# Optimization experiments

Measured on AMD Instinct MI355X. Metric: run time of the kernel, lower is better.

## Reference

```python
import jax, jax.numpy as jnp
import numpy as np

# constants mirroring init_kwargs
SPATIAL_STRIDE = 4
RADIUS2 = 0.5 ** 2
K = 32


def _fps(xyz, m):
    """Iterative farthest point sampling. xyz: [N,3] -> idx [m] int32 (starts at index 0, like pointnet2)."""
    n = xyz.shape[0]

    def body(i, carry):
        dist, idx = carry
        cur = xyz[idx[i]]                              # [3]
        d = jnp.sum((xyz - cur) ** 2, axis=-1)          # [N]
        dist = jnp.minimum(dist, d)
        idx = idx.at[i + 1].set(jnp.argmax(dist).astype(jnp.int32))
        return dist, idx

    dist0 = jnp.full((n,), 1e10, xyz.dtype)
    idx0 = jnp.zeros((m,), jnp.int32)
    _, idx = jax.lax.fori_loop(0, m - 1, body, (dist0, idx0))
    return idx


def setup_inputs() -> dict:
    key = jax.random.key(0)
    ks = jax.random.split(key, 5)
    B, T, N, C = 4, 8, 2048, 64
    C_IN = 2 * C + 3  # grouped feat2 + anchor feat1 + xyz displacement
    xyzs = jax.random.uniform(ks[0], (B, T, N, 3), dtype=jnp.float32)
    features = jax.random.normal(ks[1], (B, T, N, C), dtype=jnp.float32)
    w1 = jax.random.normal(ks[2], (C_IN, 128), dtype=jnp.float32) / np.sqrt(C_IN)
    w2 = jax.random.normal(ks[3], (128, 128), dtype=jnp.float32) / np.sqrt(128)
    w3 = jax.random.normal(ks[4], (128, 256), dtype=jnp.float32) / np.sqrt(128)
    return {
        "xyzs": xyzs, "features": features,
        "w1": w1, "b1": jnp.zeros((128,), jnp.float32),
        "w2": w2, "b2": jnp.zeros((128,), jnp.float32),
        "w3": w3, "b3": jnp.zeros((256,), jnp.float32),
    }


def reference(xyzs, features, w1, b1, w2, b2, w3, b3):
    B, T, N, _ = xyzs.shape
    M = N // SPATIAL_STRIDE

    # temporal replicate padding [1,1]
    xp = jnp.concatenate([xyzs[:, :1], xyzs, xyzs[:, -1:]], axis=1)        # [B,T+2,N,3]
    fp = jnp.concatenate([features[:, :1], features, features[:, -1:]], axis=1)
    # frames processed: i = 1..T (stride 1); neighbor frame = i+1
    xyz_a, xyz_n = xp[:, 1:T + 1], xp[:, 2:T + 2]                          # [B,T,N,3]
    feat_a, feat_n = fp[:, 1:T + 1], fp[:, 2:T + 2]                        # [B,T,N,C]

    gather = jax.vmap(jax.vmap(lambda a, i: a[i]))  # over (B, T)

    # FPS on each anchor frame
    idx = jax.vmap(jax.vmap(lambda p: _fps(p, M)))(xyz_a)                  # [B,T,M]
    anchor = gather(xyz_a, idx)                                            # [B,T,M,3]
    f1 = gather(feat_a, idx)                                               # [B,T,M,C]

    # knn of anchors into next frame, with ball-query radius clamp
    d = jnp.sum((anchor[:, :, :, None, :] - xyz_n[:, :, None, :, :]) ** 2, axis=-1)  # [B,T,M,N]
    negd, idxk = jax.lax.top_k(-d, K)                                      # [B,T,M,K]
    idxk = jnp.where(-negd <= RADIUS2, idxk, idxk[..., :1])                # duplicate nearest outside radius

    gxyz = gather(xyz_n, idxk)                                             # [B,T,M,K,3]
    gf2 = gather(feat_n, idxk)                                             # [B,T,M,K,C]
    disp = gxyz - anchor[:, :, :, None, :]
    h = jnp.concatenate(
        [gf2, jnp.broadcast_to(f1[:, :, :, None, :], gf2.shape), disp], axis=-1)  # [B,T,M,K,2C+3]

    h = jax.nn.relu(h @ w1 + b1)
    h = jax.nn.relu(h @ w2 + b2)
    h = jax.nn.relu(h @ w3 + b3)
    new_features = jnp.max(h, axis=3)                                      # [B,T,M,256]
    return anchor, new_features
```

## Files before the change

### kernel.cpp

```cpp
#include <hip/hip_runtime.h>

#define BB 4
#define TT 8
#define NN 2048
#define CC 64
#define MM 512
#define KK 32
#define H3DIM 256
#define RAD2 0.25f
#define FINF 3.4e38f

typedef _Float16 f16x8 __attribute__((ext_vector_type(8)));
typedef _Float16 f16x4 __attribute__((ext_vector_type(4)));
typedef float f32x4 __attribute__((ext_vector_type(4)));

template <int CTRL>
__device__ __forceinline__ float dpp_max_step(float x) {
    int xi = __builtin_bit_cast(int, x);
    int yi = __builtin_amdgcn_update_dpp(xi, xi, CTRL, 0xf, 0xf, false);
    return fmaxf(x, __builtin_bit_cast(float, yi));
}
__device__ __forceinline__ float wave_max64(float x) {
    x = dpp_max_step<0x111>(x);
    x = dpp_max_step<0x112>(x);
    x = dpp_max_step<0x114>(x);
    x = dpp_max_step<0x118>(x);
    x = dpp_max_step<0x142>(x);
    x = dpp_max_step<0x143>(x);
    return __builtin_bit_cast(float, __builtin_amdgcn_readlane(__builtin_bit_cast(int, x), 63));
}
template <int CTRL>
__device__ __forceinline__ unsigned long long dpp_minkey_step(unsigned long long k) {
    int lo = (int)(unsigned)k;
    int hi = (int)(unsigned)(k >> 32);
    int slo = __builtin_amdgcn_update_dpp(lo, lo, CTRL, 0xf, 0xf, false);
    int shi = __builtin_amdgcn_update_dpp(hi, hi, CTRL, 0xf, 0xf, false);
    unsigned long long s = ((unsigned long long)(unsigned)shi << 32) | (unsigned)slo;
    return s < k ? s : k;
}
__device__ __forceinline__ unsigned long long wave_minkey(unsigned long long k) {
    k = dpp_minkey_step<0x111>(k);
    k = dpp_minkey_step<0x112>(k);
    k = dpp_minkey_step<0x114>(k);
    k = dpp_minkey_step<0x118>(k);
    k = dpp_minkey_step<0x142>(k);
    k = dpp_minkey_step<0x143>(k);
    int lo = __builtin_amdgcn_readlane((int)(unsigned)k, 63);
    int hi = __builtin_amdgcn_readlane((int)(unsigned)(k >> 32), 63);
    return ((unsigned long long)(unsigned)hi << 32) | (unsigned)lo;
}

__global__ __launch_bounds__(256) void k_fps(const float* __restrict__ xyzs,
                                             int* __restrict__ fps_idx) {
    int bt = blockIdx.x;
    int tid = threadIdx.x;
    int lane = tid & 63, w = tid >> 6;
    __shared__ float sx[NN], sy[NN], sz[NN];
    __shared__ float4 rec_xyzd[2][4];
    __shared__ __align__(16) int rec_p[2][4];
    const float* src = xyzs + (size_t)bt * NN * 3;
    for (int i = tid; i < NN; i += 256) {
        sx[i] = src[i * 3 + 0];
        sy[i] = src[i * 3 + 1];
        sz[i] = src[i * 3 + 2];
    }
    __syncthreads();

    float px[8], py[8], pz[8], dist[8];
#pragma unroll
    for (int j = 0; j < 8; ++j) {
        int p = tid * 8 + j;
        px[j] = sx[p]; py[j] = sy[p]; pz[j] = sz[p];
        dist[j] = 1e10f;
    }

    if (tid == 0) fps_idx[bt * MM + 0] = 0;
    int pbase = tid * 8;
    float cx = sx[0], cy = sy[0], cz = sz[0];

    for (int it = 1; it < MM; ++it) {
        float nd[8];
#pragma unroll
        for (int j = 0; j < 8; ++j) {
            float dx = px[j] - cx, dy = py[j] - cy, dz = pz[j] - cz;
            float d = dx * dx + dy * dy + dz * dz;
            nd[j] = fminf(dist[j], d);
            dist[j] = nd[j];
        }
        float gd0 = nd[0]; int gj0 = 0;
#pragma unroll
        for (int j = 1; j < 4; ++j) if (nd[j] > gd0) { gd0 = nd[j]; gj0 = j; }
        float gd1 = nd[4]; int gj1 = 4;
#pragma unroll
        for (int j = 5; j < 8; ++j) if (nd[j] > gd1) { gd1 = nd[j]; gj1 = j; }
        bool gt = gd1 > gd0;
        float bestd = gt ? gd1 : gd0;
        int bestj = gt ? gj1 : gj0;
        int bestp = pbase + bestj;
        float wmax = wave_max64(bestd);
        unsigned long long mask = __ballot(bestd == wmax);
        int wl = __ffsll(mask) - 1;
        int wbp = __builtin_amdgcn_readlane(bestp, wl);
        if (lane == wl) {
            bool b0 = (bestj & 1) != 0, b1 = (bestj & 2) != 0, b2 = (bestj & 4) != 0;
            float x01 = b0 ? px[1] : px[0], x23 = b0 ? px[3] : px[2];
            float x45 = b0 ? px[5] : px[4], x67 = b0 ? px[7] : px[6];
            float y01 = b0 ? py[1] : py[0], y23 = b0 ? py[3] : py[2];
            float y45 = b0 ? py[5] : py[4], y67 = b0 ? py[7] : py[6];
            float z01 = b0 ? pz[1] : pz[0], z23 = b0 ? pz[3] : pz[2];
            float z45 = b0 ? pz[5] : pz[4], z67 = b0 ? pz[7] : pz[6];
            float x0123 = b1 ? x23 : x01, x4567 = b1 ? x67 : x45;
            float y0123 = b1 ? y23 : y01, y4567 = b1 ? y67 : y45;
            float z0123 = b1 ? z23 : z01, z4567 = b1 ? z67 : z45;
            float4 r;
            r.x = b2 ? x4567 : x0123;
            r.y = b2 ? y4567 : y0123;
            r.z = b2 ? z4567 : z0123;
            r.w = wmax;
            rec_xyzd[it & 1][w] = r;
        }
        if (lane == 0) rec_p[it & 1][w] = wbp;
        __syncthreads();
        float4 r0 = rec_xyzd[it & 1][0];
        float4 r1 = rec_xyzd[it & 1][1];
        float4 r2 = rec_xyzd[it & 1][2];
        float4 r3 = rec_xyzd[it & 1][3];
        int4 pv = *(const int4*)&rec_p[it & 1][0];
        bool t01 = r1.w > r0.w, t23 = r3.w > r2.w;
        float4 ra = t01 ? r1 : r0; int pa = t01 ? pv.y : pv.x;
        float4 rb = t23 ? r3 : r2; int pb = t23 ? pv.w : pv.z;
        bool tf = rb.w > ra.w;
        float4 rf = tf ? rb : ra;
        int pf = tf ? pb : pa;
        cx = rf.x; cy = rf.y; cz = rf.z;
        if (tid == 0) fps_idx[bt * MM + it] = pf;
    }
}

__global__ __launch_bounds__(256) void k_pp(const float* __restrict__ xyzs,
                                            const float* __restrict__ feats,
                                            const float* __restrict__ w1,
                                            _Float16* __restrict__ Pp) {
    __shared__ float sw[68 * 128];
    __shared__ float sin_[64 * 68];
    int tid = threadIdx.x;
    for (int i = tid; i < 68 * 128; i += 256) {
        int r = i >> 7, c = i & 127;
        float v = 0.f;
        if (r < 64) v = w1[r * 128 + c];
        else if (r < 67) v = w1[(128 + r - 64) * 128 + c];
        sw[i] = v;
    }
    int row0 = blockIdx.x * 64;
    int bt = row0 >> 11;
    int b = bt >> 3, t = bt & 7;
    int tn = (t + 1 < TT) ? (t + 1) : (TT - 1);
    size_t nbase = (size_t)(b * TT + tn) * NN + (row0 & (NN - 1));
    const float* fsrc = feats + nbase * CC;
    const float* xsrc = xyzs + nbase * 3;
    for (int i = tid; i < 1024; i += 256) {
        float4 v = ((const float4*)fsrc)[i];
        int r = i >> 4, c = (i & 15) * 4;
        *(float4*)&sin_[r * 68 + c] = v;
    }
    if (tid < 192) {
        int r = tid / 3, c = tid - r * 3;
        sin_[r * 68 + 64 + c] = xsrc[tid];
    }
    if (tid < 64) sin_[tid * 68 + 67] = 0.f;
    __syncthreads();

    int rowg = tid >> 5, colg = tid & 31;
    float4 acc[8];
#pragma unroll
    for (int i = 0; i < 8; ++i) acc[i] = make_float4(0.f, 0.f, 0.f, 0.f);
    for (int k = 0; k < 68; k += 4) {
        float4 a4[8], b4[4];
#pragma unroll
        for (int i = 0; i < 8; ++i) a4[i] = *(const float4*)&sin_[(rowg * 8 + i) * 68 + k];
#pragma unroll
        for (int kk = 0; kk < 4; ++kk) b4[kk] = *(const float4*)&sw[(k + kk) * 128 + colg * 4];
#pragma unroll
        for (int i = 0; i < 8; ++i) {
#pragma unroll
            for (int kk = 0; kk < 4; ++kk) {
                float av = (kk == 0) ? a4[i].x : (kk == 1) ? a4[i].y : (kk == 2) ? a4[i].z : a4[i].w;
                acc[i].x += av * b4[kk].x;
                acc[i].y += av * b4[kk].y;
                acc[i].z += av * b4[kk].z;
                acc[i].w += av * b4[kk].w;
            }
        }
    }
#pragma unroll
    for (int i = 0; i < 8; ++i) {
        f16x4 h;
        h[0] = (_Float16)acc[i].x; h[1] = (_Float16)acc[i].y;
        h[2] = (_Float16)acc[i].z; h[3] = (_Float16)acc[i].w;
        *(f16x4*)&Pp[(size_t)(row0 + rowg * 8 + i) * 128 + colg * 4] = h;
    }
}

__global__ __launch_bounds__(256) void k_qp(const float* __restrict__ xyzs,
                                            const float* __restrict__ feats,
                                            const float* __restrict__ w1,
                                            const float* __restrict__ b1,
                                            const int* __restrict__ fps_idx,
                                            float* __restrict__ Qp,
                                            float* __restrict__ out_anchor) {
    __shared__ float sw[68 * 128];
    __shared__ float sin_[64 * 68];
    __shared__ float sb[128];
    int tid = threadIdx.x;
    for (int i = tid; i < 68 * 128; i += 256) {
        int r = i >> 7, c = i & 127;
        float v = 0.f;
        if (r < 64) v = w1[(64 + r) * 128 + c];
        else if (r < 67) v = w1[(128 + r - 64) * 128 + c];
        sw[i] = v;
    }
    if (tid < 128) sb[tid] = b1[tid];
    int row0 = blockIdx.x * 64;
    int bt = row0 >> 9;
    size_t fbase = (size_t)bt * NN;
    {
        int r = tid >> 2, seg = tid & 3;
        int aidx = fps_idx[row0 + r];
        const float4* fr = (const float4*)(feats + (fbase + aidx) * CC);
#pragma unroll
        for (int i = 0; i < 4; ++i) {
            float4 v = fr[seg * 4 + i];
            *(float4*)&sin_[r * 68 + seg * 16 + i * 4] = v;
        }
    }
    if (tid < 64) {
        int aidx = fps_idx[row0 + tid];
        const float* xs = xyzs + (fbase + aidx) * 3;
        float x = xs[0], y = xs[1], z = xs[2];
        sin_[tid * 68 + 64] = -x;
        sin_[tid * 68 + 65] = -y;
        sin_[tid * 68 + 66] = -z;
        sin_[tid * 68 + 67] = 0.f;
        out_anchor[(size_t)(row0 + tid) * 3 + 0] = x;
        out_anchor[(size_t)(row0 + tid) * 3 + 1] = y;
        out_anchor[(size_t)(row0 + tid) * 3 + 2] = z;
    }
    __syncthreads();

    int rowg = tid >> 5, colg = tid & 31;
    float4 bias = *(const float4*)&sb[colg * 4];
    float4 acc[8];
#pragma unroll
    for (int i = 0; i < 8; ++i) acc[i] = bias;
    for (int k = 0; k < 68; k += 4) {
        float4 a4[8], b4[4];
#pragma unroll
        for (int i = 0; i < 8; ++i) a4[i] = *(const float4*)&sin_[(rowg * 8 + i) * 68 + k];
#pragma unroll
        for (int kk = 0; kk < 4; ++kk) b4[kk] = *(const float4*)&sw[(k + kk) * 128 + colg * 4];
#pragma unroll
        for (int i = 0; i < 8; ++i) {
#pragma unroll
            for (int kk = 0; kk < 4; ++kk) {
                float av = (kk == 0) ? a4[i].x : (kk == 1) ? a4[i].y : (kk == 2) ? a4[i].z : a4[i].w;
                acc[i].x += av * b4[kk].x;
                acc[i].y += av * b4[kk].y;
                acc[i].z += av * b4[kk].z;
                acc[i].w += av * b4[kk].w;
            }
        }
    }
#pragma unroll
    for (int i = 0; i < 8; ++i)
        *(float4*)&Qp[(size_t)(row0 + rowg * 8 + i) * 128 + colg * 4] = acc[i];
}

__global__ __launch_bounds__(256) void k_knn(const float* __restrict__ xyzs,
                                             const float* __restrict__ anchors,
                                             int* __restrict__ idxk) {
    __shared__ float sx[NN], sy[NN], sz[NN];
    int tid = threadIdx.x;
    int wave = tid >> 6, lane = tid & 63;
    int bt = blockIdx.x >> 6;
    int sub = blockIdx.x & 63;
    int b = bt >> 3, t = bt & 7;
    int tn = (t + 1 < TT) ? (t + 1) : (TT - 1);
    const float* src = xyzs + ((size_t)(b * TT + tn)) * NN * 3;
    for (int i = tid; i < NN; i += 256) {
        sx[i] = src[i * 3 + 0];
        sy[i] = src[i * 3 + 1];
        sz[i] = src[i * 3 + 2];
    }
    __syncthreads();

    for (int a = 0; a < 2; ++a) {
        int mrow = bt * MM + sub * 8 + wave * 2 + a;
        float ax = anchors[mrow * 3 + 0];
        float ay = anchors[mrow * 3 + 1];
        float az = anchors[mrow * 3 + 2];
        float d[32];
#pragma unroll
        for (int j = 0; j < 32; ++j) {
            int p = j * 64 + lane;
            float dx = sx[p] - ax, dy = sy[p] - ay, dz = sz[p] - az;
            d[j] = dx * dx + dy * dy + dz * dz;
        }
        int p0 = 0;
        int myidx = 0;
        for (int r = 0; r < KK; ++r) {
            float gd[4];
            int gp[4];
#pragma unroll
            for (int g = 0; g < 4; ++g) {
                gd[g] = d[g * 8];
                gp[g] = (g * 8) * 64 + lane;
#pragma unroll
                for (int jj = 1; jj < 8; ++jj) {
                    float dj = d[g * 8 + jj];
                    if (dj < gd[g]) { gd[g] = dj; gp[g] = (g * 8 + jj) * 64 + lane; }
                }
            }
            bool u01 = gd[1] < gd[0], u23 = gd[3] < gd[2];
            float da = u01 ? gd[1] : gd[0], db = u23 ? gd[3] : gd[2];
            int pa = u01 ? gp[1] : gp[0], pb = u23 ? gp[3] : gp[2];
            bool uf = db < da;
            float bd = uf ? db : da;
            int bp = uf ? pb : pa;
            unsigned long long key =
                ((unsigned long long)(unsigned)__builtin_bit_cast(unsigned, bd) << 32) |
                (unsigned)bp;
            unsigned long long wkey = wave_minkey(key);
            int pstar = (int)(unsigned)wkey;
            float dstar = __builtin_bit_cast(float, (unsigned)(wkey >> 32));
            if (r == 0) { p0 = pstar; myidx = pstar; }
            int outp = (dstar <= RAD2) ? pstar : p0;
            if (lane == r) myidx = outp;
            if (r < KK - 1) {
                int lanew = pstar & 63;
                int jw = pstar >> 6;
                bool imw = (lane == lanew);
#pragma unroll
                for (int j = 0; j < 32; ++j)
                    d[j] = (imw && j == jw) ? FINF : d[j];
            }
        }
        if (lane < KK) idxk[(size_t)mrow * KK + lane] = myidx;
    }
}

#define SM_W2 0
#define SM_W3 32768
#define SM_H1 98304
#define SM_H2 114688
#define SM_B2 131072
#define SM_B3 131584
#define SM_TOTAL 132608

__global__ __launch_bounds__(512, 1) void k_mlp(const _Float16* __restrict__ Pp,
                                                const float* __restrict__ Qp,
                                                const int* __restrict__ idxk,
                                                const float* __restrict__ w2,
                                                const float* __restrict__ b2,
                                                const float* __restrict__ w3,
                                                const float* __restrict__ b3,
                                                float* __restrict__ out_feat) {
    extern __shared__ char smem[];
    int tid = threadIdx.x;
    int bid = blockIdx.x;

    for (int i = tid; i < 128 * 128; i += 512) {
        int n = i & 127, kk = i >> 7;
        _Float16 v = (_Float16)w2[kk * 128 + n];
        *(_Float16*)(smem + SM_W2 + n * 256 + ((2 * kk) ^ ((n & 7) << 4))) = v;
    }
    for (int i = tid; i < 256 * 128; i += 512) {
        int n = i & 255, kk = i >> 8;
        _Float16 v = (_Float16)w3[kk * 256 + n];
        *(_Float16*)(smem + SM_W3 + n * 256 + ((2 * kk) ^ ((n & 7) << 4))) = v;
    }
    if (tid < 128) *(float*)(smem + SM_B2 + tid * 4) = b2[tid];
    if (tid < 256) *(float*)(smem + SM_B3 + tid * 4) = b3[tid];
    __syncthreads();

    int lane = tid & 63;
    int w = tid >> 6;
    int wm = w >> 2, wn = w & 3;
    int l15 = lane & 15, g = lane >> 4;
    int hswz = (l15 & 7) << 4;

    const f32x4 zero4 = {0.f, 0.f, 0.f, 0.f};

    for (int c = 0; c < 32; ++c) {
        int a0 = bid * 64 + c * 2;
        int bt = a0 >> 9;

        {
            int r = tid >> 3, seg = tid & 7;
            int arow = a0 + (r >> 5);
            int kidx = r & 31;
            int nk = idxk[(size_t)arow * KK + kidx];
            const _Float16* ps = Pp + ((size_t)(bt * NN + nk)) * 128 + seg * 16;
            const float* qs = Qp + (size_t)arow * 128 + seg * 16;
            int rowbase = SM_H1 + r * 256;
            int swz = (r & 7) << 4;
#pragma unroll
            for (int i = 0; i < 2; ++i) {
                f16x8 pv = *(const f16x8*)(ps + i * 8);
                f32x4 q0 = *(const f32x4*)(qs + i * 8);
                f32x4 q1 = *(const f32x4*)(qs + i * 8 + 4);
                f16x8 hv;
#pragma unroll
                for (int j = 0; j < 4; ++j) hv[j] = (_Float16)fmaxf((float)pv[j] + q0[j], 0.f);
#pragma unroll
                for (int j = 0; j < 4; ++j) hv[4 + j] = (_Float16)fmaxf((float)pv[4 + j] + q1[j], 0.f);
                *(f16x8*)(smem + rowbase + ((seg * 32 + i * 16) ^ swz)) = hv;
            }
        }
        __syncthreads();

        f32x4 acc2[2][2];
#pragma unroll
        for (int m = 0; m < 2; ++m)
#pragma unroll
            for (int n = 0; n < 2; ++n) acc2[m][n] = zero4;

#pragma unroll
        for (int ks = 0; ks < 4; ++ks) {
            int kbyte = ks * 64 + g * 16;
            f16x8 af[2], bf[2];
#pragma unroll
            for (int m = 0; m < 2; ++m) {
                int row = wm * 32 + m * 16 + l15;
                af[m] = *(const f16x8*)(smem + SM_H1 + row * 256 + (kbyte ^ hswz));
            }
#pragma unroll
            for (int n = 0; n < 2; ++n) {
                int col = wn * 32 + n * 16 + l15;
                bf[n] = *(const f16x8*)(smem + SM_W2 + col * 256 + (kbyte ^ hswz));
            }
#pragma unroll
            for (int m = 0; m < 2; ++m)
#pragma unroll
                for (int n = 0; n < 2; ++n)
                    acc2[m][n] = __builtin_amdgcn_mfma_f32_16x16x32_f16(af[m], bf[n], acc2[m][n], 0, 0, 0);
        }
#pragma unroll
        for (int m = 0; m < 2; ++m)
#pragma unroll
            for (int n = 0; n < 2; ++n) {
                int col = wn * 32 + n * 16 + l15;
                float bb = *(const float*)(smem + SM_B2 + col * 4);
#pragma unroll
                for (int r = 0; r < 4; ++r) {
                    int row = wm * 32 + m * 16 + g * 4 + r;
                    float v = fmaxf(acc2[m][n][r] + bb, 0.f);
                    *(_Float16*)(smem + SM_H2 + row * 256 + ((2 * col) ^ ((row & 7) << 4))) = (_Float16)v;
                }
            }
        __syncthreads();

        f32x4 acc3[2][4];
#pragma unroll
        for (int m = 0; m < 2; ++m)
#pragma unroll
            for (int n = 0; n < 4; ++n) acc3[m][n] = zero4;

#pragma unroll
        for (int ks = 0; ks < 4; ++ks) {
            int kbyte = ks * 64 + g * 16;
            f16x8 af[2], bf[4];
#pragma unroll
            for (int m = 0; m < 2; ++m) {
                int row = wm * 32 + m * 16 + l15;
                af[m] = *(const f16x8*)(smem + SM_H2 + row * 256 + (kbyte ^ hswz));
            }
#pragma unroll
            for (int n = 0; n < 4; ++n) {
                int col = wn * 64 + n * 16 + l15;
                bf[n] = *(const f16x8*)(smem + SM_W3 + col * 256 + (kbyte ^ hswz));
            }
#pragma unroll
            for (int m = 0; m < 2; ++m)
#pragma unroll
                for (int n = 0; n < 4; ++n)
                    acc3[m][n] = __builtin_amdgcn_mfma_f32_16x16x32_f16(af[m], bf[n], acc3[m][n], 0, 0, 0);
        }
#pragma unroll
        for (int n = 0; n < 4; ++n) {
            int col = wn * 64 + n * 16 + l15;
            float s = acc3[0][n][0];
#pragma unroll
            for (int r = 1; r < 4; ++r) s = fmaxf(s, acc3[0][n][r]);
#pragma unroll
            for (int r = 0; r < 4; ++r) s = fmaxf(s, acc3[1][n][r]);
            s = fmaxf(s, __shfl_xor(s, 16));
            s = fmaxf(s, __shfl_xor(s, 32));
            if (g == 0) {
                float bb = *(const float*)(smem + SM_B3 + col * 4);
                out_feat[(size_t)(a0 + wm) * H3DIM + col] = fmaxf(s + bb, 0.f);
            }
        }
        __syncthreads();
    }
}

extern "C" void kernel_launch(void* const* d_in, const int* in_sizes, int n_in,
                              void* d_out, int out_size, void* d_ws, size_t ws_size,
                              hipStream_t stream) {
    const float* xyzs  = (const float*)d_in[0];
    const float* feats = (const float*)d_in[1];
    const float* w1 = (const float*)d_in[2];
    const float* b1 = (const float*)d_in[3];
    const float* w2 = (const float*)d_in[4];
    const float* b2 = (const float*)d_in[5];
    const float* w3 = (const float*)d_in[6];
    const float* b3 = (const float*)d_in[7];

    float* out_anchor = (float*)d_out;
    float* out_feat = out_anchor + (size_t)BB * TT * MM * 3;

    char* ws = (char*)d_ws;
    int* fps_idx = (int*)ws;
    int* idxk = (int*)(ws + 65536);
    _Float16* Pp = (_Float16*)(ws + 65536 + 2097152);
    float* Qp = (float*)(ws + 65536 + 2097152 + 16777216);
    if (ws_size < (size_t)(65536 + 2097152 + 16777216) + (size_t)BB * TT * MM * 128 * 4)
        return;

    k_fps<<<BB * TT, 256, 0, stream>>>(xyzs, fps_idx);
    k_pp<<<BB * TT * NN / 64, 256, 0, stream>>>(xyzs, feats, w1, Pp);
    k_qp<<<BB * TT * MM / 64, 256, 0, stream>>>(xyzs, feats, w1, b1, fps_idx, Qp, out_anchor);
    k_knn<<<BB * TT * 64, 256, 0, stream>>>(xyzs, out_anchor, idxk);

    (void)hipFuncSetAttribute((const void*)k_mlp, hipFuncAttributeMaxDynamicSharedMemorySize, SM_TOTAL);
    k_mlp<<<256, 512, SM_TOTAL, stream>>>(Pp, Qp, idxk, w2, b2, w3, b3, out_feat);
}
```

Baseline: 622.1 us.

## Pack four FPS clouds per 1024-thread block and carry winner coordinates

The farthest-point-sampling kernel now processes four point clouds per 1024-thread block, with dynamic LDS holding all four clouds' coordinates, instead of one cloud per 256-thread block. The per-thread argmax now carries the winning point's xyz and index alongside the distance. This replaces the readlane and the bit-select chain the winning lane used to fetch its coordinates. The cost is that every iteration's barrier now spans 16 waves on one CU instead of 4, and the kernel uses fewer CUs, which may lengthen the serial loop's latency.

```diff
diff --git a/kernel.cpp b/kernel.cpp
--- a/kernel.cpp
+++ b/kernel.cpp
@@ -50,33 +50,43 @@
     return ((unsigned long long)(unsigned)hi << 32) | (unsigned)lo;
 }
 
-__global__ __launch_bounds__(256) void k_fps(const float* __restrict__ xyzs,
-                                             int* __restrict__ fps_idx) {
-    int bt = blockIdx.x;
+#define FPS_XYZ_F (4 * NN)
+#define FPS_REC_OFF (3 * FPS_XYZ_F * 4)
+#define FPS_LDS (FPS_REC_OFF + 2 * 16 * 16 + 2 * 16 * 4)
+
+__global__ __launch_bounds__(1024) void k_fps(const float* __restrict__ xyzs,
+                                              int* __restrict__ fps_idx) {
+    extern __shared__ char fsm[];
+    float* sx = (float*)fsm;
+    float* sy = sx + FPS_XYZ_F;
+    float* sz = sy + FPS_XYZ_F;
+    float4* recx = (float4*)(fsm + FPS_REC_OFF);
+    int* recp = (int*)(fsm + FPS_REC_OFF + 2 * 16 * 16);
+
     int tid = threadIdx.x;
-    int lane = tid & 63, w = tid >> 6;
-    __shared__ float sx[NN], sy[NN], sz[NN];
-    __shared__ float4 rec_xyzd[2][4];
-    __shared__ __align__(16) int rec_p[2][4];
-    const float* src = xyzs + (size_t)bt * NN * 3;
-    for (int i = tid; i < NN; i += 256) {
-        sx[i] = src[i * 3 + 0];
-        sy[i] = src[i * 3 + 1];
-        sz[i] = src[i * 3 + 2];
+    int cl = tid >> 8, ctid = tid & 255;
+    int lane = tid & 63, wc = (tid >> 6) & 3;
+    int cloud = blockIdx.x * 4 + cl;
+
+    const float* src = xyzs + (size_t)cloud * NN * 3;
+    for (int i = ctid; i < NN; i += 256) {
+        sx[cl * NN + i] = src[i * 3 + 0];
+        sy[cl * NN + i] = src[i * 3 + 1];
+        sz[cl * NN + i] = src[i * 3 + 2];
     }
     __syncthreads();
 
     float px[8], py[8], pz[8], dist[8];
 #pragma unroll
     for (int j = 0; j < 8; ++j) {
-        int p = tid * 8 + j;
-        px[j] = sx[p]; py[j] = sy[p]; pz[j] = sz[p];
+        int p = ctid * 8 + j;
+        px[j] = sx[cl * NN + p]; py[j] = sy[cl * NN + p]; pz[j] = sz[cl * NN + p];
         dist[j] = 1e10f;
     }
 
-    if (tid == 0) fps_idx[bt * MM + 0] = 0;
-    int pbase = tid * 8;
-    float cx = sx[0], cy = sy[0], cz = sz[0];
+    if (ctid == 0) fps_idx[cloud * MM + 0] = 0;
+    int pbase = ctid * 8;
+    float cx = sx[cl * NN], cy = sy[cl * NN], cz = sz[cl * NN];
 
     for (int it = 1; it < MM; ++it) {
         float nd[8];
@@ -87,45 +97,35 @@
             nd[j] = fminf(dist[j], d);
             dist[j] = nd[j];
         }
-        float gd0 = nd[0]; int gj0 = 0;
-#pragma unroll
-        for (int j = 1; j < 4; ++j) if (nd[j] > gd0) { gd0 = nd[j]; gj0 = j; }
-        float gd1 = nd[4]; int gj1 = 4;
-#pragma unroll
-        for (int j = 5; j < 8; ++j) if (nd[j] > gd1) { gd1 = nd[j]; gj1 = j; }
+        float gd0 = nd[0], gx0 = px[0], gy0 = py[0], gz0 = pz[0]; int gp0 = pbase;
+#pragma unroll
+        for (int j = 1; j < 4; ++j)
+            if (nd[j] > gd0) { gd0 = nd[j]; gp0 = pbase + j; gx0 = px[j]; gy0 = py[j]; gz0 = pz[j]; }
+        float gd1 = nd[4], gx1 = px[4], gy1 = py[4], gz1 = pz[4]; int gp1 = pbase + 4;
+#pragma unroll
+        for (int j = 5; j < 8; ++j)
+            if (nd[j] > gd1) { gd1 = nd[j]; gp1 = pbase + j; gx1 = px[j]; gy1 = py[j]; gz1 = pz[j]; }
         bool gt = gd1 > gd0;
         float bestd = gt ? gd1 : gd0;
-        int bestj = gt ? gj1 : gj0;
-        int bestp = pbase + bestj;
+        int   bestp = gt ? gp1 : gp0;
+        float bx = gt ? gx1 : gx0;
+        float by = gt ? gy1 : gy0;
+        float bz = gt ? gz1 : gz0;
         float wmax = wave_max64(bestd);
         unsigned long long mask = __ballot(bestd == wmax);
-        int wl = __ffsll(mask) - 1;
-        int wbp = __builtin_amdgcn_readlane(bestp, wl);
-        if (lane == wl) {
-            bool b0 = (bestj & 1) != 0, b1 = (bestj & 2) != 0, b2 = (bestj & 4) != 0;
-            float x01 = b0 ? px[1] : px[0], x23 = b0 ? px[3] : px[2];
-            float x45 = b0 ? px[5] : px[4], x67 = b0 ? px[7] : px[6];
-            float y01 = b0 ? py[1] : py[0], y23 = b0 ? py[3] : py[2];
-            float y45 = b0 ? py[5] : py[4], y67 = b0 ? py[7] : py[6];
-            float z01 = b0 ? pz[1] : pz[0], z23 = b0 ? pz[3] : pz[2];
-            float z45 = b0 ? pz[5] : pz[4], z67 = b0 ? pz[7] : pz[6];
-            float x0123 = b1 ? x23 : x01, x4567 = b1 ? x67 : x45;
-            float y0123 = b1 ? y23 : y01, y4567 = b1 ? y67 : y45;
-            float z0123 = b1 ? z23 : z01, z4567 = b1 ? z67 : z45;
-            float4 r;
-            r.x = b2 ? x4567 : x0123;
-            r.y = b2 ? y4567 : y0123;
-            r.z = b2 ? z4567 : z0123;
-            r.w = wmax;
-            rec_xyzd[it & 1][w] = r;
-        }
-        if (lane == 0) rec_p[it & 1][w] = wbp;
+        unsigned long long lower = mask & ((1ull << lane) - 1ull);
+        if ((bestd == wmax) && lower == 0ull) {
+            float4 r; r.x = bx; r.y = by; r.z = bz; r.w = wmax;
+            recx[(it & 1) * 16 + cl * 4 + wc] = r;
+            recp[(it & 1) * 16 + cl * 4 + wc] = bestp;
+        }
         __syncthreads();
-        float4 r0 = rec_xyzd[it & 1][0];
-        float4 r1 = rec_xyzd[it & 1][1];
-        float4 r2 = rec_xyzd[it & 1][2];
-        float4 r3 = rec_xyzd[it & 1][3];
-        int4 pv = *(const int4*)&rec_p[it & 1][0];
+        int rb_ = (it & 1) * 16 + cl * 4;
+        float4 r0 = recx[rb_ + 0];
+        float4 r1 = recx[rb_ + 1];
+        float4 r2 = recx[rb_ + 2];
+        float4 r3 = recx[rb_ + 3];
+        int4 pv = *(const int4*)&recp[rb_];
         bool t01 = r1.w > r0.w, t23 = r3.w > r2.w;
         float4 ra = t01 ? r1 : r0; int pa = t01 ? pv.y : pv.x;
         float4 rb = t23 ? r3 : r2; int pb = t23 ? pv.w : pv.z;
@@ -133,7 +133,7 @@
         float4 rf = tf ? rb : ra;
         int pf = tf ? pb : pa;
         cx = rf.x; cy = rf.y; cz = rf.z;
-        if (tid == 0) fps_idx[bt * MM + it] = pf;
+        if (ctid == 0) fps_idx[cloud * MM + it] = pf;
     }
 }
 
@@ -527,7 +527,8 @@
     if (ws_size < (size_t)(65536 + 2097152 + 16777216) + (size_t)BB * TT * MM * 128 * 4)
         return;
 
-    k_fps<<<BB * TT, 256, 0, stream>>>(xyzs, fps_idx);
+    (void)hipFuncSetAttribute((const void*)k_fps, hipFuncAttributeMaxDynamicSharedMemorySize, FPS_LDS);
+    k_fps<<<BB * TT / 4, 1024, FPS_LDS, stream>>>(xyzs, fps_idx);
     k_pp<<<BB * TT * NN / 64, 256, 0, stream>>>(xyzs, feats, w1, Pp);
     k_qp<<<BB * TT * MM / 64, 256, 0, stream>>>(xyzs, feats, w1, b1, fps_idx, Qp, out_anchor);
     k_knn<<<BB * TT * 64, 256, 0, stream>>>(xyzs, out_anchor, idxk);
```

Measured after the change: 837.2 us. +34.6%, slower.

## Fuse FPS and point-projection kernels into one launch to overlap serial FPS

Applied to the files above, without the earlier changes.

Merges the serial FPS kernel (32 blocks) and the per-point W1 projection kernel into a single launch, with blocks indexed by role. The aim is to let the projection GEMM fill idle CUs while the long serial FPS loop runs. The FPS inner loop is also simplified to a single running argmax and reads the new centre from LDS by index instead of passing coordinates through shared memory. KNN now reads anchor coordinates via fps_idx directly, so it no longer depends on k_qp and is launched before it. Trade-offs: both block roles share one larger dynamic-LDS allocation, which may lower occupancy for the projection blocks, and there is an extra LDS read on each FPS iteration's critical path.

```diff
diff --git a/kernel.cpp b/kernel.cpp
--- a/kernel.cpp
+++ b/kernel.cpp
@@ -50,154 +50,131 @@
     return ((unsigned long long)(unsigned)hi << 32) | (unsigned)lo;
 }
 
-__global__ __launch_bounds__(256) void k_fps(const float* __restrict__ xyzs,
-                                             int* __restrict__ fps_idx) {
-    int bt = blockIdx.x;
+#define FPP_LDS 52224
+
+__global__ __launch_bounds__(256) void k_fps_pp(const float* __restrict__ xyzs,
+                                                const float* __restrict__ feats,
+                                                const float* __restrict__ w1,
+                                                int* __restrict__ fps_idx,
+                                                _Float16* __restrict__ Pp) {
+    extern __shared__ char fsm[];
     int tid = threadIdx.x;
-    int lane = tid & 63, w = tid >> 6;
-    __shared__ float sx[NN], sy[NN], sz[NN];
-    __shared__ float4 rec_xyzd[2][4];
-    __shared__ __align__(16) int rec_p[2][4];
-    const float* src = xyzs + (size_t)bt * NN * 3;
-    for (int i = tid; i < NN; i += 256) {
-        sx[i] = src[i * 3 + 0];
-        sy[i] = src[i * 3 + 1];
-        sz[i] = src[i * 3 + 2];
-    }
-    __syncthreads();
-
-    float px[8], py[8], pz[8], dist[8];
-#pragma unroll
-    for (int j = 0; j < 8; ++j) {
-        int p = tid * 8 + j;
-        px[j] = sx[p]; py[j] = sy[p]; pz[j] = sz[p];
-        dist[j] = 1e10f;
-    }
-
-    if (tid == 0) fps_idx[bt * MM + 0] = 0;
-    int pbase = tid * 8;
-    float cx = sx[0], cy = sy[0], cz = sz[0];
-
-    for (int it = 1; it < MM; ++it) {
-        float nd[8];
+
+    if (blockIdx.x < BB * TT) {
+        float* sx = (float*)fsm;
+        float* sy = sx + NN;
+        float* sz = sy + NN;
+        float* pd = sz + NN;
+        int* pi = (int*)(pd + 8);
+        int bt = blockIdx.x;
+        int lane = tid & 63, w = tid >> 6;
+        const float* src = xyzs + (size_t)bt * NN * 3;
+        for (int i = tid; i < NN; i += 256) {
+            sx[i] = src[i * 3 + 0];
+            sy[i] = src[i * 3 + 1];
+            sz[i] = src[i * 3 + 2];
+        }
+        __syncthreads();
+
+        float px[8], py[8], pz[8], dist[8];
 #pragma unroll
         for (int j = 0; j < 8; ++j) {
-            float dx = px[j] - cx, dy = py[j] - cy, dz = pz[j] - cz;
-            float d = dx * dx + dy * dy + dz * dz;
-            nd[j] = fminf(dist[j], d);
-            dist[j] = nd[j];
-        }
-        float gd0 = nd[0]; int gj0 = 0;
-#pragma unroll
-        for (int j = 1; j < 4; ++j) if (nd[j] > gd0) { gd0 = nd[j]; gj0 = j; }
-        float gd1 = nd[4]; int gj1 = 4;
-#pragma unroll
-        for (int j = 5; j < 8; ++j) if (nd[j] > gd1) { gd1 = nd[j]; gj1 = j; }
-        bool gt = gd1 > gd0;
-        float bestd = gt ? gd1 : gd0;
-        int bestj = gt ? gj1 : gj0;
-        int bestp = pbase + bestj;
-        float wmax = wave_max64(bestd);
-        unsigned long long mask = __ballot(bestd == wmax);
-        int wl = __ffsll(mask) - 1;
-        int wbp = __builtin_amdgcn_readlane(bestp, wl);
-        if (lane == wl) {
-            bool b0 = (bestj & 1) != 0, b1 = (bestj & 2) != 0, b2 = (bestj & 4) != 0;
-            float x01 = b0 ? px[1] : px[0], x23 = b0 ? px[3] : px[2];
-            float x45 = b0 ? px[5] : px[4], x67 = b0 ? px[7] : px[6];
-            float y01 = b0 ? py[1] : py[0], y23 = b0 ? py[3] : py[2];
-            float y45 = b0 ? py[5] : py[4], y67 = b0 ? py[7] : py[6];
-            float z01 = b0 ? pz[1] : pz[0], z23 = b0 ? pz[3] : pz[2];
-            float z45 = b0 ? pz[5] : pz[4], z67 = b0 ? pz[7] : pz[6];
-            float x0123 = b1 ? x23 : x01, x4567 = b1 ? x67 : x45;
-            float y0123 = b1 ? y23 : y01, y4567 = b1 ? y67 : y45;
-            float z0123 = b1 ? z23 : z01, z4567 = b1 ? z67 : z45;
-            float4 r;
-            r.x = b2 ? x4567 : x0123;
-            r.y = b2 ? y4567 : y0123;
-            r.z = b2 ? z4567 : z0123;
-            r.w = wmax;
-            rec_xyzd[it & 1][w] = r;
-        }
-        if (lane == 0) rec_p[it & 1][w] = wbp;
+            int p = tid * 8 + j;
+            px[j] = sx[p]; py[j] = sy[p]; pz[j] = sz[p];
+            dist[j] = 1e10f;
+        }
+
+        int cur = 0;
+        if (tid == 0) fps_idx[bt * MM + 0] = 0;
+        int pbase = tid * 8;
+
+        for (int it = 1; it < MM; ++it) {
+            float cx = sx[cur], cy = sy[cur], cz = sz[cur];
+            float bestd = -1.0f;
+            int bestp = 0;
+#pragma unroll
+            for (int j = 0; j < 8; ++j) {
+                float dx = px[j] - cx, dy = py[j] - cy, dz = pz[j] - cz;
+                float d = dx * dx + dy * dy + dz * dz;
+                float nd = fminf(dist[j], d);
+                dist[j] = nd;
+                if (nd > bestd) { bestd = nd; bestp = pbase + j; }
+            }
+            float wmax = wave_max64(bestd);
+            unsigned long long mask = __ballot(bestd == wmax);
+            int wl = __ffsll(mask) - 1;
+            int wbp = __builtin_amdgcn_readlane(bestp, wl);
+            if (lane == 0) { pd[(it & 1) * 4 + w] = wmax; pi[(it & 1) * 4 + w] = wbp; }
+            __syncthreads();
+            float bd = pd[(it & 1) * 4 + 0];
+            int bp = pi[(it & 1) * 4 + 0];
+#pragma unroll
+            for (int q = 1; q < 4; ++q) {
+                float d2 = pd[(it & 1) * 4 + q];
+                int p2 = pi[(it & 1) * 4 + q];
+                if (d2 > bd) { bd = d2; bp = p2; }
+            }
+            cur = bp;
+            if (tid == 0) fps_idx[bt * MM + it] = cur;
+        }
+    } else {
+        float* sw = (float*)fsm;
+        float* sin_ = sw + 68 * 128;
+        for (int i = tid; i < 68 * 128; i += 256) {
+            int r = i >> 7, c = i & 127;
+            float v = 0.f;
+            if (r < 64) v = w1[r * 128 + c];
+            else if (r < 67) v = w1[(128 + r - 64) * 128 + c];
+            sw[i] = v;
+        }
+        int row0 = (blockIdx.x - BB * TT) * 64;
+        int bt = row0 >> 11;
+        int b = bt >> 3, t = bt & 7;
+        int tn = (t + 1 < TT) ? (t + 1) : (TT - 1);
+        size_t nbase = (size_t)(b * TT + tn) * NN + (row0 & (NN - 1));
+        const float* fsrc = feats + nbase * CC;
+        const float* xsrc = xyzs + nbase * 3;
+        for (int i = tid; i < 1024; i += 256) {
+            float4 v = ((const float4*)fsrc)[i];
+            int r = i >> 4, c = (i & 15) * 4;
+            *(float4*)&sin_[r * 68 + c] = v;
+        }
+        if (tid < 192) {
+            int r = tid / 3, c = tid - r * 3;
+            sin_[r * 68 + 64 + c] = xsrc[tid];
+        }
+        if (tid < 64) sin_[tid * 68 + 67] = 0.f;
         __syncthreads();
-        float4 r0 = rec_xyzd[it & 1][0];
-        float4 r1 = rec_xyzd[it & 1][1];
-        float4 r2 = rec_xyzd[it & 1][2];
-        float4 r3 = rec_xyzd[it & 1][3];
-        int4 pv = *(const int4*)&rec_p[it & 1][0];
-        bool t01 = r1.w > r0.w, t23 = r3.w > r2.w;
-        float4 ra = t01 ? r1 : r0; int pa = t01 ? pv.y : pv.x;
-        float4 rb = t23 ? r3 : r2; int pb = t23 ? pv.w : pv.z;
-        bool tf = rb.w > ra.w;
-        float4 rf = tf ? rb : ra;
-        int pf = tf ? pb : pa;
-        cx = rf.x; cy = rf.y; cz = rf.z;
-        if (tid == 0) fps_idx[bt * MM + it] = pf;
-    }
-}
-
-__global__ __launch_bounds__(256) void k_pp(const float* __restrict__ xyzs,
-                                            const float* __restrict__ feats,
-                                            const float* __restrict__ w1,
-                                            _Float16* __restrict__ Pp) {
-    __shared__ float sw[68 * 128];
-    __shared__ float sin_[64 * 68];
-    int tid = threadIdx.x;
-    for (int i = tid; i < 68 * 128; i += 256) {
-        int r = i >> 7, c = i & 127;
-        float v = 0.f;
-        if (r < 64) v = w1[r * 128 + c];
-        else if (r < 67) v = w1[(128 + r - 64) * 128 + c];
-        sw[i] = v;
-    }
-    int row0 = blockIdx.x * 64;
-    int bt = row0 >> 11;
-    int b = bt >> 3, t = bt & 7;
-    int tn = (t + 1 < TT) ? (t + 1) : (TT - 1);
-    size_t nbase = (size_t)(b * TT + tn) * NN + (row0 & (NN - 1));
-    const float* fsrc = feats + nbase * CC;
-    const float* xsrc = xyzs + nbase * 3;
-    for (int i = tid; i < 1024; i += 256) {
-        float4 v = ((const float4*)fsrc)[i];
-        int r = i >> 4, c = (i & 15) * 4;
-        *(float4*)&sin_[r * 68 + c] = v;
-    }
-    if (tid < 192) {
-        int r = tid / 3, c = tid - r * 3;
-        sin_[r * 68 + 64 + c] = xsrc[tid];
-    }
-    if (tid < 64) sin_[tid * 68 + 67] = 0.f;
-    __syncthreads();
-
-    int rowg = tid >> 5, colg = tid & 31;
-    float4 acc[8];
-#pragma unroll
-    for (int i = 0; i < 8; ++i) acc[i] = make_float4(0.f, 0.f, 0.f, 0.f);
-    for (int k = 0; k < 68; k += 4) {
-        float4 a4[8], b4[4];
-#pragma unroll
-        for (int i = 0; i < 8; ++i) a4[i] = *(const float4*)&sin_[(rowg * 8 + i) * 68 + k];
-#pragma unroll
-        for (int kk = 0; kk < 4; ++kk) b4[kk] = *(const float4*)&sw[(k + kk) * 128 + colg * 4];
+
+        int rowg = tid >> 5, colg = tid & 31;
+        float4 acc[8];
+#pragma unroll
+        for (int i = 0; i < 8; ++i) acc[i] = make_float4(0.f, 0.f, 0.f, 0.f);
+        for (int k = 0; k < 68; k += 4) {
+            float4 a4[8], b4[4];
+#pragma unroll
+            for (int i = 0; i < 8; ++i) a4[i] = *(const float4*)&sin_[(rowg * 8 + i) * 68 + k];
+#pragma unroll
+            for (int kk = 0; kk < 4; ++kk) b4[kk] = *(const float4*)&sw[(k + kk) * 128 + colg * 4];
+#pragma unroll
+            for (int i = 0; i < 8; ++i) {
+#pragma unroll
+                for (int kk = 0; kk < 4; ++kk) {
+                    float av = (kk == 0) ? a4[i].x : (kk == 1) ? a4[i].y : (kk == 2) ? a4[i].z : a4[i].w;
+                    acc[i].x += av * b4[kk].x;
+                    acc[i].y += av * b4[kk].y;
+                    acc[i].z += av * b4[kk].z;
+                    acc[i].w += av * b4[kk].w;
+                }
+            }
+        }
 #pragma unroll
         for (int i = 0; i < 8; ++i) {
-#pragma unroll
-            for (int kk = 0; kk < 4; ++kk) {
-                float av = (kk == 0) ? a4[i].x : (kk == 1) ? a4[i].y : (kk == 2) ? a4[i].z : a4[i].w;
-                acc[i].x += av * b4[kk].x;
-                acc[i].y += av * b4[kk].y;
-                acc[i].z += av * b4[kk].z;
-                acc[i].w += av * b4[kk].w;
-            }
-        }
-    }
-#pragma unroll
-    for (int i = 0; i < 8; ++i) {
-        f16x4 h;
-        h[0] = (_Float16)acc[i].x; h[1] = (_Float16)acc[i].y;
-        h[2] = (_Float16)acc[i].z; h[3] = (_Float16)acc[i].w;
-        *(f16x4*)&Pp[(size_t)(row0 + rowg * 8 + i) * 128 + colg * 4] = h;
+            f16x4 h;
+            h[0] = (_Float16)acc[i].x; h[1] = (_Float16)acc[i].y;
+            h[2] = (_Float16)acc[i].z; h[3] = (_Float16)acc[i].w;
+            *(f16x4*)&Pp[(size_t)(row0 + rowg * 8 + i) * 128 + colg * 4] = h;
+        }
     }
 }
 
@@ -276,7 +253,7 @@
 }
 
 __global__ __launch_bounds__(256) void k_knn(const float* __restrict__ xyzs,
-                                             const float* __restrict__ anchors,
+                                             const int* __restrict__ fps_idx,
                                              int* __restrict__ idxk) {
     __shared__ float sx[NN], sy[NN], sz[NN];
     int tid = threadIdx.x;
@@ -295,9 +272,9 @@
 
     for (int a = 0; a < 2; ++a) {
         int mrow = bt * MM + sub * 8 + wave * 2 + a;
-        float ax = anchors[mrow * 3 + 0];
-        float ay = anchors[mrow * 3 + 1];
-        float az = anchors[mrow * 3 + 2];
+        int aidx = fps_idx[mrow];
+        const float* xs = xyzs + ((size_t)bt * NN + aidx) * 3;
+        float ax = xs[0], ay = xs[1], az = xs[2];
         float d[32];
 #pragma unroll
         for (int j = 0; j < 32; ++j) {
@@ -527,10 +504,10 @@
     if (ws_size < (size_t)(65536 + 2097152 + 16777216) + (size_t)BB * TT * MM * 128 * 4)
         return;
 
-    k_fps<<<BB * TT, 256, 0, stream>>>(xyzs, fps_idx);
-    k_pp<<<BB * TT * NN / 64, 256, 0, stream>>>(xyzs, feats, w1, Pp);
+    (void)hipFuncSetAttribute((const void*)k_fps_pp, hipFuncAttributeMaxDynamicSharedMemorySize, FPP_LDS);
+    k_fps_pp<<<BB * TT + BB * TT * NN / 64, 256, FPP_LDS, stream>>>(xyzs, feats, w1, fps_idx, Pp);
+    k_knn<<<BB * TT * 64, 256, 0, stream>>>(xyzs, fps_idx, idxk);
     k_qp<<<BB * TT * MM / 64, 256, 0, stream>>>(xyzs, feats, w1, b1, fps_idx, Qp, out_anchor);
-    k_knn<<<BB * TT * 64, 256, 0, stream>>>(xyzs, out_anchor, idxk);
 
     (void)hipFuncSetAttribute((const void*)k_mlp, hipFuncAttributeMaxDynamicSharedMemorySize, SM_TOTAL);
     k_mlp<<<256, 512, SM_TOTAL, stream>>>(Pp, Qp, idxk, w2, b2, w3, b3, out_feat);
```

After: 543.1 us. 1.15x faster.
